# Optimization experiments

Hardware: AMD Instinct MI355X
Metric: run time of the kernel (lower is better)

The kernel has to match this reference:

```python
import jax, jax.numpy as jnp
import numpy as np

EPS = 1e-6        # RMSNorm140 eps
LAM = 0.1         # lambda_: second-order score weight
HAD = 0.05        # hadamard_scale

def _rmsnorm(x, w):
    return x * jax.lax.rsqrt(jnp.mean(x * x, axis=-1, keepdims=True) + EPS) * w

def _rope(x):
    # x: [b, h, s, d]; interleaved-pair rotary embedding (theta=10000)
    b, h, s, d = x.shape
    inv = 1.0 / (10000.0 ** (jnp.arange(0, d, 2, dtype=jnp.float32) / d))
    ang = jnp.arange(s, dtype=jnp.float32)[:, None] * inv[None, :]  # [s, d/2]
    cos, sin = jnp.cos(ang), jnp.sin(ang)
    x1, x2 = x[..., 0::2], x[..., 1::2]
    out = jnp.stack([x1 * cos - x2 * sin, x1 * sin + x2 * cos], axis=-1)
    return out.reshape(b, h, s, d)

def _rotate_half(x):
    d = x.shape[-1] // 2
    return jnp.concatenate([-x[..., d:], x[..., :d]], axis=-1)

def _attn_pass(Q, K, V):
    # scores = (Q@K^T + lam * Q^2 @ (K^2)^T) / sqrt(head_dim)   (second-order amplify)
    scale = 1.0 / jnp.sqrt(jnp.float32(Q.shape[-1]))
    scores = (jnp.einsum('bhsd,bhtd->bhst', Q, K)
              + LAM * jnp.einsum('bhsd,bhtd->bhst', Q * Q, K * K)) * scale
    return jnp.einsum('bhst,bhtd->bhsd', jax.nn.softmax(scores, axis=-1), V)

def _attention(x, wq, wk, wv, wo, gate_w):
    b, s, dim = x.shape
    hd = gate_w.shape[0]
    nh = dim // hd
    def proj(w):  # StickyLinear: x @ W^T, W stored [out, in]
        return (x @ w.T).reshape(b, s, nh, hd).transpose(0, 2, 1, 3)  # [b,h,s,d]
    Q, K, V = proj(wq), proj(wk), proj(wv)
    Q, K = _rope(Q), _rope(K)
    out1 = _attn_pass(Q, K, V)
    # rotated second pass + per-channel sigmoid gate over head_dim
    out2 = _attn_pass(_rotate_half(Q), _rotate_half(K), V)
    g = jax.nn.sigmoid(gate_w)
    out = out1 * (1.0 - g) + out2 * g
    out = out + HAD * out * out  # Hadamard mix (elementwise nonlinearity)
    out = out.transpose(0, 2, 1, 3).reshape(b, s, dim)
    return out @ wo.T

def _ffn(x, w1, w3, w2):
    # SwiGLU: down( silu(gate(x)) * up(x) )
    return (jax.nn.silu(x @ w1.T) * (x @ w3.T)) @ w2.T

def reference(x, norm1_w, norm2_w, wq, wk, wv, wo, gate_w, w1, w3, w2):
    h = x + _attention(_rmsnorm(x, norm1_w), wq, wk, wv, wo, gate_w)
    return h + _ffn(_rmsnorm(h, norm2_w), w1, w3, w2)

def setup_inputs() -> dict:
    B, S, D, NH, DFF = 2, 1024, 2048, 16, 8192
    HD = D // NH
    key = jax.random.key(0)
    ks = jax.random.split(key, 9)
    std = 0.02
    return {
        'x': jax.random.normal(ks[0], (B, S, D), dtype=jnp.float32),
        'norm1_w': jnp.ones((D,), jnp.float32),
        'norm2_w': jnp.ones((D,), jnp.float32),
        'wq': jax.random.normal(ks[1], (D, D), jnp.float32) * std,
        'wk': jax.random.normal(ks[2], (D, D), jnp.float32) * std,
        'wv': jax.random.normal(ks[3], (D, D), jnp.float32) * std,
        'wo': jax.random.normal(ks[4], (D, D), jnp.float32) * std,
        'gate_w': jax.random.normal(ks[5], (HD,), jnp.float32) * 0.01,
        'w1': jax.random.normal(ks[6], (DFF, D), jnp.float32) * std,
        'w3': jax.random.normal(ks[7], (DFF, D), jnp.float32) * std,
        'w2': jax.random.normal(ks[8], (D, DFF), jnp.float32) * std,
    }
```

## Files before the change

kernel.cpp:

```cpp
#include <hip/hip_runtime.h>
#include <hip/hip_bf16.h>

typedef unsigned short u16;
typedef unsigned int u32;
typedef u16 u16x8 __attribute__((ext_vector_type(8)));
typedef float f32x4 __attribute__((ext_vector_type(4)));

__device__ __forceinline__ u16 f2bf(float f) {
  union { float f; u32 u; } v; v.f = f;
  u32 r = v.u + 0x7FFFu + ((v.u >> 16) & 1u);
  return (u16)(r >> 16);
}
__device__ __forceinline__ float bf2f(u16 h) {
  union { u32 u; float f; } v; v.u = ((u32)h) << 16;
  return v.f;
}
__device__ __forceinline__ void mfma_bf16_16x16x32(f32x4& acc, const f32x4& a, const f32x4& b) {
  asm("v_mfma_f32_16x16x32_bf16 %0, %1, %2, %0" : "+v"(acc) : "v"(a), "v"(b));
}
__device__ __forceinline__ void gload_lds16(const void* g, void* l) {
  __builtin_amdgcn_global_load_lds(
      (const __attribute__((address_space(1))) unsigned int*)g,
      (__attribute__((address_space(3))) unsigned int*)l, 16, 0, 0);
}

__global__ __launch_bounds__(256) void cvt_k(const float* __restrict__ src,
                                             u16* __restrict__ dst, int n8) {
  int i = blockIdx.x * 256 + threadIdx.x;
  if (i >= n8) return;
  float4 f0 = *(const float4*)&src[(size_t)i * 8];
  float4 f1 = *(const float4*)&src[(size_t)i * 8 + 4];
  u16x8 o;
  o[0] = f2bf(f0.x); o[1] = f2bf(f0.y); o[2] = f2bf(f0.z); o[3] = f2bf(f0.w);
  o[4] = f2bf(f1.x); o[5] = f2bf(f1.y); o[6] = f2bf(f1.z); o[7] = f2bf(f1.w);
  *(u16x8*)&dst[(size_t)i * 8] = o;
}

__global__ __launch_bounds__(256) void cvt13_k(const float* __restrict__ src,
                                               u16* __restrict__ dst, int half) {
  int r = blockIdx.x;
  int dr = ((r >> 4) << 5) + (r & 15) + (half << 4);
  int t = threadIdx.x;
  const float* s = src + (size_t)r * 2048 + t * 8;
  float4 f0 = *(const float4*)s;
  float4 f1 = *(const float4*)(s + 4);
  u16x8 o;
  o[0] = f2bf(f0.x); o[1] = f2bf(f0.y); o[2] = f2bf(f0.z); o[3] = f2bf(f0.w);
  o[4] = f2bf(f1.x); o[5] = f2bf(f1.y); o[6] = f2bf(f1.z); o[7] = f2bf(f1.w);
  *(u16x8*)&dst[(size_t)dr * 2048 + t * 8] = o;
}

__global__ __launch_bounds__(256) void rmsnorm_k(const float* __restrict__ X,
                                                 const float* __restrict__ W,
                                                 u16* __restrict__ O) {
  const int row = blockIdx.x;
  const int tid = threadIdx.x;
  const float* x = X + (size_t)row * 2048;
  float4 v0 = *(const float4*)&x[tid * 8];
  float4 v1 = *(const float4*)&x[tid * 8 + 4];
  float s = v0.x * v0.x + v0.y * v0.y + v0.z * v0.z + v0.w * v0.w
          + v1.x * v1.x + v1.y * v1.y + v1.z * v1.z + v1.w * v1.w;
  #pragma unroll
  for (int m = 1; m < 64; m <<= 1) s += __shfl_xor(s, m);
  __shared__ float red[4];
  if ((tid & 63) == 0) red[tid >> 6] = s;
  __syncthreads();
  float tot = red[0] + red[1] + red[2] + red[3];
  float r = rsqrtf(tot * (1.0f / 2048.0f) + 1e-6f);
  float4 w0 = *(const float4*)&W[tid * 8];
  float4 w1 = *(const float4*)&W[tid * 8 + 4];
  u16x8 o;
  o[0] = f2bf(v0.x * r * w0.x); o[1] = f2bf(v0.y * r * w0.y);
  o[2] = f2bf(v0.z * r * w0.z); o[3] = f2bf(v0.w * r * w0.w);
  o[4] = f2bf(v1.x * r * w1.x); o[5] = f2bf(v1.y * r * w1.y);
  o[6] = f2bf(v1.z * r * w1.z); o[7] = f2bf(v1.w * r * w1.w);
  *(u16x8*)&O[(size_t)row * 2048 + tid * 8] = o;
}

#define EPI_F32 0
#define EPI_ADDF32 1
#define EPI_SWIGLU 2

template <int EPI>
__global__ __launch_bounds__(256) void gemm_bt(const u16* __restrict__ A,
                                               const u16* __restrict__ B,
                                               float* __restrict__ Cf,
                                               u16* __restrict__ Cb,
                                               const float* __restrict__ R,
                                               int M, int N, int Kt,
                                               int lda, int ldb) {
  __shared__ __align__(16) u16 As[2][128 * 32];
  __shared__ __align__(16) u16 Bs[2][128 * 32];
  const int tid = threadIdx.x;
  const int lane = tid & 63;
  const int w = tid >> 6;
  const int wm = w >> 1, wn = w & 1;
  const int m0 = blockIdx.y * 128, n0 = blockIdx.x * 128;
  const int z = blockIdx.z;
  A += (size_t)z * Kt;
  B += (size_t)z * Kt;
  Cf += (size_t)z * M * N;
  const int r0 = tid >> 2;
  const int c0 = (tid & 3) * 8;
  const int r1 = r0 + 64;
  const int laneM = lane & 15;
  const int laneK = (lane >> 4) * 8;

  f32x4 acc[4][4];
  #pragma unroll
  for (int i = 0; i < 4; i++)
    #pragma unroll
    for (int j = 0; j < 4; j++) acc[i][j] = (f32x4){0.f, 0.f, 0.f, 0.f};

  const u16* Ar0 = &A[(size_t)(m0 + r0) * lda + c0];
  const u16* Ar1 = &A[(size_t)(m0 + r1) * lda + c0];
  const u16* Br0 = &B[(size_t)(n0 + r0) * ldb + c0];
  const u16* Br1 = &B[(size_t)(n0 + r1) * ldb + c0];
  const int lofs0 = r0 * 32 + c0;
  const int lofs1 = r1 * 32 + c0;

  auto stage = [&](int bsel, int kt) {
    gload_lds16(Ar0 + kt, &As[bsel][lofs0]);
    gload_lds16(Ar1 + kt, &As[bsel][lofs1]);
    gload_lds16(Br0 + kt, &Bs[bsel][lofs0]);
    gload_lds16(Br1 + kt, &Bs[bsel][lofs1]);
  };

  stage(0, 0);
  const int nt = Kt >> 5;
  for (int t = 0; t < nt; t++) {
    const int cur = t & 1;
    if (t + 1 < nt) {
      stage(cur ^ 1, (t + 1) << 5);
      asm volatile("s_waitcnt vmcnt(4)" ::: "memory");
    } else {
      asm volatile("s_waitcnt vmcnt(0)" ::: "memory");
    }
    __builtin_amdgcn_s_barrier();
    __builtin_amdgcn_sched_barrier(0);
    f32x4 af[4], bfr[4];
    #pragma unroll
    for (int mi = 0; mi < 4; mi++)
      af[mi] = *(const f32x4*)&As[cur][(wm * 64 + mi * 16 + laneM) * 32 + laneK];
    #pragma unroll
    for (int ni = 0; ni < 4; ni++)
      bfr[ni] = *(const f32x4*)&Bs[cur][(wn * 64 + ni * 16 + laneM) * 32 + laneK];
    #pragma unroll
    for (int mi = 0; mi < 4; mi++)
      #pragma unroll
      for (int ni = 0; ni < 4; ni++)
        mfma_bf16_16x16x32(acc[mi][ni], af[mi], bfr[ni]);
    __builtin_amdgcn_sched_barrier(0);
    __builtin_amdgcn_s_barrier();
  }

  const int rowb = (lane >> 4) * 4;
  const int coll = lane & 15;
  #pragma unroll
  for (int mi = 0; mi < 4; mi++) {
    #pragma unroll
    for (int i = 0; i < 4; i++) {
      int row = m0 + wm * 64 + mi * 16 + rowb + i;
      if constexpr (EPI == EPI_SWIGLU) {
        #pragma unroll
        for (int ni = 0; ni < 4; ni += 2) {
          float g = acc[mi][ni][i];
          float u = acc[mi][ni + 1][i];
          float sg = g / (1.0f + __expf(-g));
          int j = (n0 >> 1) + wn * 32 + (ni >> 1) * 16 + coll;
          Cb[(size_t)row * (N >> 1) + j] = f2bf(sg * u);
        }
      } else {
        #pragma unroll
        for (int ni = 0; ni < 4; ni++) {
          int col = n0 + wn * 64 + ni * 16 + coll;
          size_t idx = (size_t)row * N + col;
          float v = acc[mi][ni][i];
          if constexpr (EPI == EPI_F32) Cf[idx] = v;
          else Cf[idx] = v + R[idx];
        }
      }
    }
  }
}

__global__ __launch_bounds__(256) void reduce5_k(const float* __restrict__ P,
                                                 const float* __restrict__ H,
                                                 float* __restrict__ out) {
  size_t i = ((size_t)blockIdx.x * 256 + threadIdx.x) * 4;
  const size_t MN = 4194304;
  float4 a = *(const float4*)&P[i];
  float4 b = *(const float4*)&P[MN + i];
  float4 c = *(const float4*)&P[2 * MN + i];
  float4 d = *(const float4*)&P[3 * MN + i];
  float4 h = *(const float4*)&H[i];
  float4 o;
  o.x = a.x + b.x + c.x + d.x + h.x;
  o.y = a.y + b.y + c.y + d.y + h.y;
  o.z = a.z + b.z + c.z + d.z + h.z;
  o.w = a.w + b.w + c.w + d.w + h.w;
  *(float4*)&out[i] = o;
}

__device__ __forceinline__ void rope_row(const float* __restrict__ src,
                                         u16* __restrict__ dst, int s, int q4) {
  float vv[32];
  #pragma unroll
  for (int t = 0; t < 8; t++) {
    float4 f = *(const float4*)&src[t * 4];
    vv[t * 4] = f.x; vv[t * 4 + 1] = f.y; vv[t * 4 + 2] = f.z; vv[t * 4 + 3] = f.w;
  }
  u16 o1[32], o2[32];
  #pragma unroll
  for (int jl = 0; jl < 16; jl++) {
    int j = q4 * 16 + jl;
    float inv = exp2f(-(float)j * 0.20762050593046014f);
    float ang = (float)s * inv;
    float sn, cs;
    __sincosf(ang, &sn, &cs);
    float a = vv[2 * jl], b = vv[2 * jl + 1];
    float r1 = a * cs - b * sn;
    float r2 = a * sn + b * cs;
    o1[2 * jl] = f2bf(r1);
    o1[2 * jl + 1] = f2bf(r2);
    o2[2 * jl] = f2bf(0.31622776601683794f * r1 * r1);
    o2[2 * jl + 1] = f2bf(0.31622776601683794f * r2 * r2);
  }
  #pragma unroll
  for (int t = 0; t < 4; t++) {
    *(u16x8*)&dst[q4 * 32 + t * 8] = *(const u16x8*)&o1[t * 8];
    *(u16x8*)&dst[128 + q4 * 32 + t * 8] = *(const u16x8*)&o2[t * 8];
  }
}

__global__ __launch_bounds__(256) void qkv_post_k(const float* __restrict__ QKVF,
                                                  u16* __restrict__ Qe,
                                                  u16* __restrict__ Ke,
                                                  u16* __restrict__ Vt) {
  const int st = blockIdx.x;
  const int bh = blockIdx.y;
  const int b = bh >> 4, h = bh & 15;
  const int tid = threadIdx.x;
  {
    int r = tid >> 2, q4 = tid & 3;
    int s = st * 64 + r;
    size_t rowin = ((size_t)b * 1024 + s) * 6144 + h * 128 + q4 * 32;
    size_t rowe = ((size_t)bh * 1024 + s) * 256;
    rope_row(QKVF + rowin, Qe + rowe, s, q4);
    rope_row(QKVF + rowin + 2048, Ke + rowe, s, q4);
  }
  __shared__ __align__(16) u16 vts[128 * 72];
  {
    int r = tid >> 2, q4 = tid & 3;
    int s = st * 64 + r;
    const float* src = QKVF + ((size_t)b * 1024 + s) * 6144 + 4096 + h * 128 + q4 * 32;
    #pragma unroll
    for (int k = 0; k < 32; k += 4) {
      float4 f = *(const float4*)&src[k];
      int d = q4 * 32 + k;
      vts[(d + 0) * 72 + r] = f2bf(f.x);
      vts[(d + 1) * 72 + r] = f2bf(f.y);
      vts[(d + 2) * 72 + r] = f2bf(f.z);
      vts[(d + 3) * 72 + r] = f2bf(f.w);
    }
  }
  __syncthreads();
  {
    int d = tid >> 1, sp = (tid & 1) * 32;
    u16* dst = Vt + ((size_t)bh * 128 + d) * 1024 + st * 64 + sp;
    #pragma unroll
    for (int k = 0; k < 32; k += 8)
      *(u16x8*)&dst[k] = *(const u16x8*)&vts[d * 72 + sp + k];
  }
}

__global__ __launch_bounds__(256, 2) void attn_k(const u16* __restrict__ Qe,
                                                 const u16* __restrict__ Ke,
                                                 const u16* __restrict__ Vt,
                                                 u16* __restrict__ AO) {
  const int bh = blockIdx.x;
  const int qt = blockIdx.y;
  const int b = bh >> 4, h = bh & 15;
  const int tid = threadIdx.x;
  const int w = tid >> 6, lane = tid & 63;
  const int laneM = lane & 15, laneG = lane >> 4;

  __shared__ __align__(16) char smem[57344];
  u16* plu = (u16*)(smem + 49152 + w * 2048);

  const char* KeB = (const char*)Ke + (size_t)bh * 524288;
  const char* VtB = (const char*)Vt + (size_t)bh * 262144;

  const size_t qbase = ((size_t)bh * 1024 + qt * 64 + w * 16 + laneM) * 256 + laneG * 8;
  f32x4 qf[8];
  #pragma unroll
  for (int kk = 0; kk < 8; kk++) qf[kk] = *(const f32x4*)&Qe[qbase + kk * 32];

  float m_i[4], l_i[4];
  #pragma unroll
  for (int i = 0; i < 4; i++) { m_i[i] = -1e30f; l_i[i] = 0.f; }
  f32x4 accO[8];
  #pragma unroll
  for (int n = 0; n < 8; n++) accO[n] = (f32x4){0.f, 0.f, 0.f, 0.f};

  u16x8 kreg[4], vreg[2];
  auto loadRegs = [&](int ktn) {
    const char* ks = KeB + (size_t)ktn * 16384;
    #pragma unroll
    for (int j = 0; j < 4; j++) {
      int p = j * 4096 + tid * 16;
      kreg[j] = *(const u16x8*)(ks + p);
    }
    const char* vs = VtB + (size_t)ktn * 64;
    #pragma unroll
    for (int j = 0; j < 2; j++) {
      int p = j * 4096 + tid * 16;
      int r = p >> 6, x = p & 63;
      vreg[j] = *(const u16x8*)(vs + (size_t)r * 2048 + x);
    }
  };
  auto writeLDS = [&](int bsel) {
    char* kd = smem + (bsel ? 16384 : 0);
    #pragma unroll
    for (int j = 0; j < 4; j++) {
      int p = j * 4096 + tid * 16;
      int r = p >> 9, x = p & 511;
      *(u16x8*)(kd + r * 512 + (x ^ ((r & 7) << 4))) = kreg[j];
    }
    char* vd = smem + 32768 + (bsel ? 8192 : 0);
    #pragma unroll
    for (int j = 0; j < 2; j++) {
      int p = j * 4096 + tid * 16;
      int r = p >> 6, x = p & 63;
      *(u16x8*)(vd + r * 64 + (x ^ (((r >> 1) & 3) << 4))) = vreg[j];
    }
  };

  loadRegs(0);
  writeLDS(0);
  int cur = 0;
  const float scale = 0.08838834764831845f;

  for (int kt = 0; kt < 32; kt++) {
    if (kt < 31) loadRegs(kt + 1);
    __syncthreads();
    const char* Kc = smem + (cur ? 16384 : 0);
    const char* Vc = smem + 32768 + (cur ? 8192 : 0);

    f32x4 accS[2];
    #pragma unroll
    for (int n = 0; n < 2; n++) accS[n] = (f32x4){0.f, 0.f, 0.f, 0.f};
    #pragma unroll
    for (int n = 0; n < 2; n++) {
      int r = n * 16 + laneM;
      const char* krow = Kc + r * 512;
      int sw = (r & 7) << 4;
      #pragma unroll
      for (int kk = 0; kk < 8; kk++) {
        f32x4 kf = *(const f32x4*)(krow + ((kk * 64 + laneG * 16) ^ sw));
        mfma_bf16_16x16x32(accS[n], qf[kk], kf);
      }
    }

    float p[2][4], sf[4];
    #pragma unroll
    for (int i = 0; i < 4; i++) {
      float mx = fmaxf(accS[0][i], accS[1][i]) * scale;
      #pragma unroll
      for (int m = 1; m < 16; m <<= 1) mx = fmaxf(mx, __shfl_xor(mx, m));
      float mnew = fmaxf(m_i[i], mx);
      sf[i] = __expf(m_i[i] - mnew);
      m_i[i] = mnew;
      float p0 = __expf(accS[0][i] * scale - mnew);
      float p1 = __expf(accS[1][i] * scale - mnew);
      p[0][i] = p0; p[1][i] = p1;
      float rs = p0 + p1;
      #pragma unroll
      for (int m = 1; m < 16; m <<= 1) rs += __shfl_xor(rs, m);
      l_i[i] = l_i[i] * sf[i] + rs;
    }
    #pragma unroll
    for (int n = 0; n < 8; n++) {
      accO[n][0] *= sf[0]; accO[n][1] *= sf[1];
      accO[n][2] *= sf[2]; accO[n][3] *= sf[3];
    }

    #pragma unroll
    for (int n = 0; n < 2; n++)
      #pragma unroll
      for (int i = 0; i < 4; i++) {
        int row = laneG * 4 + i;
        int col = n * 16 + laneM;
        plu[row * 64 + (col ^ (((row >> 2) & 3) << 4))] = f2bf(p[n][i]);
      }
    f32x4 pa = *(const f32x4*)&plu[laneM * 64 +
                                   ((laneG * 8) ^ (((laneM >> 2) & 3) << 4))];

    #pragma unroll
    for (int n = 0; n < 8; n++) {
      int r = n * 16 + laneM;
      f32x4 vf = *(const f32x4*)(Vc + r * 64 + ((laneG * 16) ^ (((r >> 1) & 3) << 4)));
      mfma_bf16_16x16x32(accO[n], pa, vf);
    }

    if (kt < 31) writeLDS(cur ^ 1);
    cur ^= 1;
  }

  #pragma unroll
  for (int i = 0; i < 4; i++) {
    float inv_l = 1.f / l_i[i];
    int row = b * 1024 + qt * 64 + w * 16 + laneG * 4 + i;
    #pragma unroll
    for (int n = 0; n < 8; n++) {
      float o = accO[n][i] * inv_l;
      o = o + 0.05f * o * o;
      AO[(size_t)row * 2048 + h * 128 + n * 16 + laneM] = f2bf(o);
    }
  }
}

extern "C" void kernel_launch(void* const* d_in, const int* in_sizes, int n_in,
                              void* d_out, int out_size, void* d_ws, size_t ws_size,
                              hipStream_t stream) {
  const float* x   = (const float*)d_in[0];
  const float* n1w = (const float*)d_in[1];
  const float* n2w = (const float*)d_in[2];
  const float* wq  = (const float*)d_in[3];
  const float* wk  = (const float*)d_in[4];
  const float* wv  = (const float*)d_in[5];
  const float* wo  = (const float*)d_in[6];
  const float* w1  = (const float*)d_in[8];
  const float* w3  = (const float*)d_in[9];
  const float* w2  = (const float*)d_in[10];

  char* ws = (char*)d_ws;
  u16* WQKVb = (u16*)(ws + 0);
  u16* WOb   = (u16*)(ws + 25165824);
  u16* W13b  = (u16*)(ws + 33554432);
  u16* W2b   = (u16*)(ws + 100663296);
  u16* XN    = (u16*)(ws + 134217728);
  float* QKVF = (float*)(ws + 142606336);
  u16* U     = (u16*)(ws + 142606336);
  float* P   = (float*)(ws + 176160768);
  u16* QE    = (u16*)(ws + 192937984);
  u16* KE    = (u16*)(ws + 209715200);
  u16* VT    = (u16*)(ws + 226492416);
  u16* AO    = (u16*)(ws + 234881024);
  float* H   = (float*)(ws + 243269632);

  cvt_k<<<2048, 256, 0, stream>>>(wq, WQKVb, 524288);
  cvt_k<<<2048, 256, 0, stream>>>(wk, WQKVb + 4194304, 524288);
  cvt_k<<<2048, 256, 0, stream>>>(wv, WQKVb + 8388608, 524288);
  cvt_k<<<2048, 256, 0, stream>>>(wo, WOb, 524288);
  cvt13_k<<<8192, 256, 0, stream>>>(w1, W13b, 0);
  cvt13_k<<<8192, 256, 0, stream>>>(w3, W13b, 1);
  cvt_k<<<8192, 256, 0, stream>>>(w2, W2b, 2097152);

  rmsnorm_k<<<2048, 256, 0, stream>>>(x, n1w, XN);

  gemm_bt<EPI_F32><<<dim3(48, 16), 256, 0, stream>>>(
      XN, WQKVb, QKVF, nullptr, nullptr, 2048, 6144, 2048, 2048, 2048);

  qkv_post_k<<<dim3(16, 32), 256, 0, stream>>>(QKVF, QE, KE, VT);

  attn_k<<<dim3(32, 16), 256, 0, stream>>>(QE, KE, VT, AO);

  gemm_bt<EPI_ADDF32><<<dim3(16, 16), 256, 0, stream>>>(
      AO, WOb, H, nullptr, x, 2048, 2048, 2048, 2048, 2048);

  rmsnorm_k<<<2048, 256, 0, stream>>>(H, n2w, XN);

  gemm_bt<EPI_SWIGLU><<<dim3(128, 16), 256, 0, stream>>>(
      XN, W13b, nullptr, U, nullptr, 2048, 16384, 2048, 2048, 2048);

  gemm_bt<EPI_F32><<<dim3(16, 16, 4), 256, 0, stream>>>(
      U, W2b, P, nullptr, nullptr, 2048, 2048, 2048, 8192, 8192);

  reduce5_k<<<4096, 256, 0, stream>>>(P, H, (float*)d_out);
}
```

Baseline: 568.7 us.

## Add 256x256-tile 512-thread GEMM with swizzled LDS and use it for big GEMMs

Adds a new GEMM kernel with 256x256 output tiles, 8 waves, BK=64, double-buffered direct-to-LDS loads with XOR swizzle, and s_setprio around the MFMA bursts. It replaces the 128-tile GEMM for the QKV projection, the SwiGLU up/gate projection and the split-K down projection. Larger tiles raise arithmetic intensity and cut global/LDS traffic per flop. In exchange they use more LDS and registers, and give fewer blocks on small grids (e.g. 192 or 256 blocks), which risks poor CU utilization.

Measured after the change: 556.0 us. -2.2%, faster.

```diff
diff --git a/kernel.cpp b/kernel.cpp
--- a/kernel.cpp
+++ b/kernel.cpp
@@ -161,23 +161,136 @@
     #pragma unroll
     for (int i = 0; i < 4; i++) {
       int row = m0 + wm * 64 + mi * 16 + rowb + i;
+      #pragma unroll
+      for (int ni = 0; ni < 4; ni++) {
+        int col = n0 + wn * 64 + ni * 16 + coll;
+        size_t idx = (size_t)row * N + col;
+        float v = acc[mi][ni][i];
+        if constexpr (EPI == EPI_F32) Cf[idx] = v;
+        else Cf[idx] = v + R[idx];
+      }
+    }
+  }
+}
+
+template <int EPI>
+__global__ __launch_bounds__(512, 2) void gemm256(const u16* __restrict__ A,
+                                                  const u16* __restrict__ B,
+                                                  float* __restrict__ Cf,
+                                                  u16* __restrict__ Cb,
+                                                  int M, int N, int Kt,
+                                                  int lda, int ldb) {
+  __shared__ __align__(16) char sm[131072];
+  const int tid = threadIdx.x;
+  const int lane = tid & 63, w = tid >> 6;
+  const int wr = w >> 2, wc = w & 3;
+  const int laneM = lane & 15, laneG = lane >> 4;
+  const int m0 = blockIdx.y * 256, n0 = blockIdx.x * 256;
+  const int z = blockIdx.z;
+  A += (size_t)z * Kt;
+  B += (size_t)z * Kt;
+  Cf += (size_t)z * M * N;
+
+  const int srow = tid >> 3;
+  const int scb = (tid & 7) * 16;
+
+  f32x4 acc[8][4];
+  #pragma unroll
+  for (int i = 0; i < 8; i++)
+    #pragma unroll
+    for (int j = 0; j < 4; j++) acc[i][j] = (f32x4){0.f, 0.f, 0.f, 0.f};
+
+  auto stage = [&](int buf, int ktE, int ht) {
+    const int half = ht & 1;
+    const bool isA = ht < 2;
+    char* base = sm + (isA ? 0 : 65536) + buf * 32768 + half * 16384;
+    const u16* src = isA ? A : B;
+    const int ld = isA ? lda : ldb;
+    const int rb = (isA ? m0 : n0) + half * 128;
+    #pragma unroll
+    for (int j = 0; j < 2; j++) {
+      int row = j * 64 + srow;
+      int scol = (scb ^ ((row & 7) << 4)) >> 1;
+      gload_lds16(src + (size_t)(rb + row) * ld + ktE + scol,
+                  base + j * 8192 + tid * 16);
+    }
+  };
+
+  const int nkt = Kt >> 6;
+  #pragma unroll
+  for (int ht = 0; ht < 4; ht++) stage(0, 0, ht);
+
+  const int bHalf = wc >> 1;
+  const int bRow0 = (wc & 1) * 64;
+
+  for (int t = 0; t < nkt; t++) {
+    const int cb_ = t & 1;
+    char* aBase = sm + cb_ * 32768 + wr * 16384;
+    char* bBase = sm + 65536 + cb_ * 32768 + bHalf * 16384;
+    if (t + 1 < nkt) {
+      #pragma unroll
+      for (int ht = 0; ht < 4; ht++) stage(cb_ ^ 1, (t + 1) << 6, ht);
+      asm volatile("s_waitcnt vmcnt(8)" ::: "memory");
+    } else {
+      asm volatile("s_waitcnt vmcnt(0)" ::: "memory");
+    }
+    __builtin_amdgcn_s_barrier();
+    #pragma unroll
+    for (int q = 0; q < 4; q++) {
+      const int mh = q >> 1, nh = q & 1;
+      f32x4 af[4][2], bg[2][2];
+      #pragma unroll
+      for (int mi = 0; mi < 4; mi++)
+        #pragma unroll
+        for (int ks = 0; ks < 2; ks++) {
+          int r = (mh * 4 + mi) * 16 + laneM;
+          int cbv = ks * 64 + laneG * 16;
+          af[mi][ks] = *(const f32x4*)(aBase + r * 128 + (cbv ^ ((r & 7) << 4)));
+        }
+      #pragma unroll
+      for (int ni = 0; ni < 2; ni++)
+        #pragma unroll
+        for (int ks = 0; ks < 2; ks++) {
+          int r = bRow0 + (nh * 2 + ni) * 16 + laneM;
+          int cbv = ks * 64 + laneG * 16;
+          bg[ni][ks] = *(const f32x4*)(bBase + r * 128 + (cbv ^ ((r & 7) << 4)));
+        }
+      if (q > 0) __builtin_amdgcn_s_barrier();
+      asm volatile("s_waitcnt lgkmcnt(0)" ::: "memory");
+      __builtin_amdgcn_sched_barrier(0);
+      __builtin_amdgcn_s_setprio(1);
+      #pragma unroll
+      for (int mi = 0; mi < 4; mi++)
+        #pragma unroll
+        for (int ni = 0; ni < 2; ni++)
+          #pragma unroll
+          for (int ks = 0; ks < 2; ks++)
+            mfma_bf16_16x16x32(acc[mh * 4 + mi][nh * 2 + ni], af[mi][ks], bg[ni][ks]);
+      __builtin_amdgcn_s_setprio(0);
+      __builtin_amdgcn_sched_barrier(0);
+      __builtin_amdgcn_s_barrier();
+    }
+  }
+
+  #pragma unroll
+  for (int mi = 0; mi < 8; mi++) {
+    #pragma unroll
+    for (int i = 0; i < 4; i++) {
+      int row = m0 + wr * 128 + mi * 16 + laneG * 4 + i;
       if constexpr (EPI == EPI_SWIGLU) {
         #pragma unroll
-        for (int ni = 0; ni < 4; ni += 2) {
-          float g = acc[mi][ni][i];
-          float u = acc[mi][ni + 1][i];
+        for (int np = 0; np < 2; np++) {
+          float g = acc[mi][np * 2][i];
+          float u = acc[mi][np * 2 + 1][i];
           float sg = g / (1.0f + __expf(-g));
-          int j = (n0 >> 1) + wn * 32 + (ni >> 1) * 16 + coll;
+          int j = (n0 >> 1) + wc * 32 + np * 16 + laneM;
           Cb[(size_t)row * (N >> 1) + j] = f2bf(sg * u);
         }
       } else {
         #pragma unroll
         for (int ni = 0; ni < 4; ni++) {
-          int col = n0 + wn * 64 + ni * 16 + coll;
-          size_t idx = (size_t)row * N + col;
-          float v = acc[mi][ni][i];
-          if constexpr (EPI == EPI_F32) Cf[idx] = v;
-          else Cf[idx] = v + R[idx];
+          int col = n0 + wc * 64 + ni * 16 + laneM;
+          Cf[(size_t)row * N + col] = acc[mi][ni][i];
         }
       }
     }
@@ -459,8 +572,8 @@
 
   rmsnorm_k<<<2048, 256, 0, stream>>>(x, n1w, XN);
 
-  gemm_bt<EPI_F32><<<dim3(48, 16), 256, 0, stream>>>(
-      XN, WQKVb, QKVF, nullptr, nullptr, 2048, 6144, 2048, 2048, 2048);
+  gemm256<EPI_F32><<<dim3(24, 8), 512, 0, stream>>>(
+      XN, WQKVb, QKVF, nullptr, 2048, 6144, 2048, 2048, 2048);
 
   qkv_post_k<<<dim3(16, 32), 256, 0, stream>>>(QKVF, QE, KE, VT);
 
@@ -471,11 +584,11 @@
 
   rmsnorm_k<<<2048, 256, 0, stream>>>(H, n2w, XN);
 
-  gemm_bt<EPI_SWIGLU><<<dim3(128, 16), 256, 0, stream>>>(
-      XN, W13b, nullptr, U, nullptr, 2048, 16384, 2048, 2048, 2048);
-
-  gemm_bt<EPI_F32><<<dim3(16, 16, 4), 256, 0, stream>>>(
-      U, W2b, P, nullptr, nullptr, 2048, 2048, 2048, 8192, 8192);
+  gemm256<EPI_SWIGLU><<<dim3(64, 8), 512, 0, stream>>>(
+      XN, W13b, nullptr, U, 2048, 16384, 2048, 2048, 2048);
+
+  gemm256<EPI_F32><<<dim3(8, 8, 4), 512, 0, stream>>>(
+      U, W2b, P, nullptr, 2048, 2048, 2048, 8192, 8192);
 
   reduce5_k<<<4096, 256, 0, stream>>>(P, H, (float*)d_out);
 }
```
